# Kernel optimization log

Measured on AMD Instinct MI355X. Metric: run time of the kernel, lower is better.

The kernel has to match this reference:

```python
import jax, jax.numpy as jnp
import numpy as np

N_NODES = 50000
N_EDGES = 600000
IN_DIM = 128
HID = 128
N_CLASSES = 40
N_GRAPHS = 128


def setup_inputs() -> dict:
    key = jax.random.key(0)
    ks = jax.random.split(key, 12)
    x = jax.random.normal(ks[0], (N_NODES, IN_DIM), dtype=jnp.float32)
    edge_index = jax.random.randint(ks[1], (2, N_EDGES), 0, N_NODES, dtype=jnp.int64)
    batch = jnp.sort(jax.random.randint(ks[2], (N_NODES,), 0, N_GRAPHS, dtype=jnp.int64))
    dims = [IN_DIM, HID, HID, N_CLASSES]
    params = {}
    for l in range(3):
        d_in, d_out = dims[l], dims[l + 1]
        s = 1.0 / np.sqrt(d_in)
        params[f"Wl{l}"] = jax.random.uniform(ks[3 + 3 * l], (d_out, d_in), jnp.float32, -s, s)
        params[f"bl{l}"] = jax.random.uniform(ks[4 + 3 * l], (d_out,), jnp.float32, -s, s)
        params[f"Wr{l}"] = jax.random.uniform(ks[5 + 3 * l], (d_out, d_in), jnp.float32, -s, s)
    return {"x": x, "edge_index": edge_index, "batch": batch, **params}


def _sage_layer(h, src, dst, Wl, bl, Wr):
    # message: relu(x_j) (edge_attr is None -> zero), mean-aggregate at dst
    m = jnp.maximum(h[src], 0.0)                       # [E, d]
    agg = jax.ops.segment_sum(m, dst, num_segments=N_NODES)
    cnt = jax.ops.segment_sum(jnp.ones((m.shape[0],), h.dtype), dst, num_segments=N_NODES)
    agg = agg / jnp.maximum(cnt, 1.0)[:, None]
    # lin_l(agg) + lin_r(x)
    return agg @ Wl.T + bl + h @ Wr.T


def reference(x, edge_index, batch, Wl0, bl0, Wr0, Wl1, bl1, Wr1, Wl2, bl2, Wr2):
    src, dst = edge_index[0], edge_index[1]
    Ws = [(Wl0, bl0, Wr0), (Wl1, bl1, Wr1), (Wl2, bl2, Wr2)]
    h = x
    for l, (Wl, bl, Wr) in enumerate(Ws):
        # dropout is identity in eval mode
        h = _sage_layer(h, src, dst, Wl, bl, Wr)
        if l != len(Ws) - 1:
            h = jnp.maximum(h, 0.0)
    # global mean pool over graphs
    gsum = jax.ops.segment_sum(h, batch, num_segments=N_GRAPHS)
    gcnt = jax.ops.segment_sum(jnp.ones((h.shape[0],), h.dtype), batch, num_segments=N_GRAPHS)
    g = gsum / jnp.maximum(gcnt, 1.0)[:, None]
    return h, g
```

## Files before the change

kernel.cpp:

```cpp
#include <hip/hip_runtime.h>
#include <hip/hip_bf16.h>


#define NODES 50000
#define K_DIM 128
#define N_GRAPHS 128

typedef __attribute__((ext_vector_type(8))) short short8;
typedef __attribute__((ext_vector_type(4))) short short4v;
typedef __attribute__((ext_vector_type(4))) float f32x4;

__device__ inline short f2bf(float f) {
    unsigned u = __builtin_bit_cast(unsigned, f);
    u += 0x7FFFu + ((u >> 16) & 1u);
    return (short)(u >> 16);
}
__device__ inline float bf2f(short h) {
    unsigned u = ((unsigned)(unsigned short)h) << 16;
    return __builtin_bit_cast(float, u);
}
__device__ inline float blo(unsigned u) { return __builtin_bit_cast(float, u << 16); }
__device__ inline float bhi(unsigned u) { return __builtin_bit_cast(float, u & 0xFFFF0000u); }
__device__ inline unsigned hilo_pack(float f) {
    short h = f2bf(f);
    short l = f2bf(f - bf2f(h));
    return ((unsigned)(unsigned short)h) | (((unsigned)(unsigned short)l) << 16);
}

__global__ void init_kernel(const float* __restrict__ w0, const float* __restrict__ w1,
                            const float* __restrict__ w2, const float* __restrict__ w3,
                            const float* __restrict__ w4, const float* __restrict__ w5,
                            short* __restrict__ whi, short* __restrict__ wlo,
                            int* __restrict__ deg, const int* __restrict__ batch,
                            int* __restrict__ gstart, int* __restrict__ counter,
                            const float* __restrict__ x, short* __restrict__ xb,
                            float* __restrict__ gsum, int N) {
    int idx = blockIdx.x * 256 + threadIdx.x;
    if (idx < N * (K_DIM / 4)) {
        float4 v = reinterpret_cast<const float4*>(x)[idx];
        short4v b;
        b[0] = f2bf(fmaxf(v.x, 0.f));
        b[1] = f2bf(fmaxf(v.y, 0.f));
        b[2] = f2bf(fmaxf(v.z, 0.f));
        b[3] = f2bf(fmaxf(v.w, 0.f));
        *reinterpret_cast<short4v*>(&xb[idx * 4]) = b;
    }
    if (idx < N) deg[idx] = 0;
    if (idx < N_GRAPHS * 40) gsum[idx] = 0.f;
    if (idx == 0) *counter = 0;
    const int TOT = 4 * 16384 + 96 * 128;
    if (idx < TOT) {
        float v;
        if (idx < 65536) {
            int m = idx >> 14, e = idx & 16383;
            const float* W = (m == 0) ? w0 : (m == 1) ? w1 : (m == 2) ? w2 : w3;
            v = W[e];
        } else {
            int i2 = idx - 65536;
            int row = i2 >> 7, col = i2 & 127;
            if (row < 40)      v = w4[row * 128 + col];
            else if (row < 80) v = w5[(row - 40) * 128 + col];
            else               v = 0.f;
        }
        unsigned p = hilo_pack(v);
        whi[idx] = (short)(p & 0xFFFFu);
        wlo[idx] = (short)(p >> 16);
    }
    if (idx <= N_GRAPHS) {
        int g = idx;
        int lo = 0, hi = N;
        while (lo < hi) {
            int mid = (lo + hi) >> 1;
            if (batch[mid] < g) lo = mid + 1; else hi = mid;
        }
        gstart[g] = lo;
    }
}

__global__ void deg_kernel(const int* __restrict__ dst, int* __restrict__ deg, int E) {
    int e = blockIdx.x * blockDim.x + threadIdx.x;
    if (e < E) atomicAdd(&deg[dst[e]], 1);
}

__global__ void csr_offsets(const int* __restrict__ deg, int* __restrict__ counter,
                            int* __restrict__ rowptr, int* __restrict__ fillpos, int N) {
    const int tid = threadIdx.x, lane = tid & 63, wv = tid >> 6;
    int i = blockIdx.x * 256 + tid;
    int v = (i < N) ? deg[i] : 0;
    int incl = v;
    #pragma unroll
    for (int off = 1; off < 64; off <<= 1) {
        int t = __shfl_up(incl, off, 64);
        if (lane >= off) incl += t;
    }
    __shared__ int ws[4];
    __shared__ int sbase;
    if (lane == 63) ws[wv] = incl;
    __syncthreads();
    if (tid == 0) sbase = atomicAdd(counter, ws[0] + ws[1] + ws[2] + ws[3]);
    __syncthreads();
    int add = sbase;
    for (int k = 0; k < wv; ++k) add += ws[k];
    int excl = add + incl - v;
    if (i < N) { rowptr[i] = excl; fillpos[i] = excl; }
}

__global__ void fill_kernel(const int* __restrict__ src, const int* __restrict__ dst,
                            int* __restrict__ fillpos, int* __restrict__ csr_src, int E) {
    int e = blockIdx.x * blockDim.x + threadIdx.x;
    if (e < E) {
        int p = atomicAdd(&fillpos[dst[e]], 1);
        csr_src[p] = src[e];
    }
}

__global__ void agg_bf16(const unsigned short* __restrict__ hb,
                         const int* __restrict__ rowptr, const int* __restrict__ deg,
                         const int* __restrict__ csr_src,
                         short* __restrict__ aggb, int N) {
    int w = (blockIdx.x * blockDim.x + threadIdx.x) >> 6;
    if (w >= N) return;
    int lane = threadIdx.x & 63;
    int slot = lane >> 4, l16 = lane & 15;
    int s = rowptr[w];
    int e = s + deg[w];
    const uint4* T = reinterpret_cast<const uint4*>(hb);
    float2 a0 = make_float2(0.f, 0.f), a1 = a0, a2 = a0, a3 = a0;
    int i = s + slot;
    for (; i + 4 < e; i += 8) {
        uint4 va = T[(size_t)csr_src[i] * 16 + l16];
        uint4 vb = T[(size_t)csr_src[i + 4] * 16 + l16];
        a0.x += blo(va.x) + blo(vb.x); a0.y += bhi(va.x) + bhi(vb.x);
        a1.x += blo(va.y) + blo(vb.y); a1.y += bhi(va.y) + bhi(vb.y);
        a2.x += blo(va.z) + blo(vb.z); a2.y += bhi(va.z) + bhi(vb.z);
        a3.x += blo(va.w) + blo(vb.w); a3.y += bhi(va.w) + bhi(vb.w);
    }
    for (; i < e; i += 4) {
        uint4 va = T[(size_t)csr_src[i] * 16 + l16];
        a0.x += blo(va.x); a0.y += bhi(va.x);
        a1.x += blo(va.y); a1.y += bhi(va.y);
        a2.x += blo(va.z); a2.y += bhi(va.z);
        a3.x += blo(va.w); a3.y += bhi(va.w);
    }
    #pragma unroll
    for (int off = 16; off <= 32; off <<= 1) {
        a0.x += __shfl_xor(a0.x, off, 64); a0.y += __shfl_xor(a0.y, off, 64);
        a1.x += __shfl_xor(a1.x, off, 64); a1.y += __shfl_xor(a1.y, off, 64);
        a2.x += __shfl_xor(a2.x, off, 64); a2.y += __shfl_xor(a2.y, off, 64);
        a3.x += __shfl_xor(a3.x, off, 64); a3.y += __shfl_xor(a3.y, off, 64);
    }
    if (slot == 0) {
        float inv = 1.0f / fmaxf((float)(e - s), 1.0f);
        short8 b;
        b[0] = f2bf(a0.x * inv); b[1] = f2bf(a0.y * inv);
        b[2] = f2bf(a1.x * inv); b[3] = f2bf(a1.y * inv);
        b[4] = f2bf(a2.x * inv); b[5] = f2bf(a2.y * inv);
        b[6] = f2bf(a3.x * inv); b[7] = f2bf(a3.y * inv);
        *reinterpret_cast<short8*>(&aggb[(size_t)w * K_DIM + l16 * 8]) = b;
    }
}

__global__ __launch_bounds__(256) void sage0_mfma(
        const short* __restrict__ Ab_in, const float* __restrict__ Xf,
        const short* __restrict__ Bhl, const short* __restrict__ Bll,
        const short* __restrict__ Bhr, const short* __restrict__ Blr,
        const float* __restrict__ bl,
        short* __restrict__ outHi, short* __restrict__ outLo, int N) {
    constexpr int BM = 64;
    constexpr int LSTR = 40;
    const int tid = threadIdx.x;
    const int lane = tid & 63;
    const int wave = tid >> 6;
    const int l15 = lane & 15;
    const int quad = lane >> 4;
    const int m0 = blockIdx.x * BM;
    const int srow = tid >> 2, sc8 = tid & 3;

    __shared__ __align__(16) short Ab [BM * LSTR];
    __shared__ __align__(16) short Ahi[BM * LSTR];
    __shared__ __align__(16) short Alo[BM * LSTR];

    f32x4 acc[4][2];
    #pragma unroll
    for (int i = 0; i < 4; ++i)
        #pragma unroll
        for (int j = 0; j < 2; ++j) acc[i][j] = (f32x4){0.f, 0.f, 0.f, 0.f};

    const short8 zero8 = (short8){0, 0, 0, 0, 0, 0, 0, 0};
    const int sm = m0 + srow;

    for (int k0 = 0; k0 < K_DIM; k0 += 32) {
        __syncthreads();
        {
            short8 va = zero8, vh = zero8, vl = zero8;
            if (sm < N) {
                va = *reinterpret_cast<const short8*>(Ab_in + (size_t)sm * K_DIM + k0 + sc8 * 8);
                const float* xp = Xf + (size_t)sm * K_DIM + k0 + sc8 * 8;
                float4 f0 = *reinterpret_cast<const float4*>(xp);
                float4 f1 = *reinterpret_cast<const float4*>(xp + 4);
                float fv[8] = {f0.x, f0.y, f0.z, f0.w, f1.x, f1.y, f1.z, f1.w};
                #pragma unroll
                for (int j = 0; j < 8; ++j) {
                    unsigned p = hilo_pack(fv[j]);
                    vh[j] = (short)(p & 0xFFFFu);
                    vl[j] = (short)(p >> 16);
                }
            }
            *reinterpret_cast<short8*>(&Ab [srow * LSTR + sc8 * 8]) = va;
            *reinterpret_cast<short8*>(&Ahi[srow * LSTR + sc8 * 8]) = vh;
            *reinterpret_cast<short8*>(&Alo[srow * LSTR + sc8 * 8]) = vl;
        }
        short8 bhl_[2], bll_[2], bhr_[2], blr_[2];
        #pragma unroll
        for (int nt = 0; nt < 2; ++nt) {
            int n = wave * 32 + nt * 16 + l15;
            size_t off = (size_t)n * K_DIM + k0 + quad * 8;
            bhl_[nt] = *reinterpret_cast<const short8*>(Bhl + off);
            bll_[nt] = *reinterpret_cast<const short8*>(Bll + off);
            bhr_[nt] = *reinterpret_cast<const short8*>(Bhr + off);
            blr_[nt] = *reinterpret_cast<const short8*>(Blr + off);
        }
        __syncthreads();
        #pragma unroll
        for (int mt = 0; mt < 4; ++mt) {
            int row = mt * 16 + l15;
            short8 ab = *reinterpret_cast<const short8*>(&Ab [row * LSTR + quad * 8]);
            short8 ah = *reinterpret_cast<const short8*>(&Ahi[row * LSTR + quad * 8]);
            short8 ao = *reinterpret_cast<const short8*>(&Alo[row * LSTR + quad * 8]);
            #pragma unroll
            for (int nt = 0; nt < 2; ++nt) {
                acc[mt][nt] = __builtin_amdgcn_mfma_f32_16x16x32_bf16(ab, bhl_[nt], acc[mt][nt], 0, 0, 0);
                acc[mt][nt] = __builtin_amdgcn_mfma_f32_16x16x32_bf16(ab, bll_[nt], acc[mt][nt], 0, 0, 0);
                acc[mt][nt] = __builtin_amdgcn_mfma_f32_16x16x32_bf16(ah, bhr_[nt], acc[mt][nt], 0, 0, 0);
                acc[mt][nt] = __builtin_amdgcn_mfma_f32_16x16x32_bf16(ah, blr_[nt], acc[mt][nt], 0, 0, 0);
                acc[mt][nt] = __builtin_amdgcn_mfma_f32_16x16x32_bf16(ao, bhr_[nt], acc[mt][nt], 0, 0, 0);
            }
        }
    }

    #pragma unroll
    for (int mt = 0; mt < 4; ++mt) {
        #pragma unroll
        for (int nt = 0; nt < 2; ++nt) {
            int col = wave * 32 + nt * 16 + l15;
            float b = bl[col];
            #pragma unroll
            for (int reg = 0; reg < 4; ++reg) {
                int row = m0 + mt * 16 + quad * 4 + reg;
                if (row < N) {
                    float v = fmaxf(acc[mt][nt][reg] + b, 0.f);
                    unsigned p = hilo_pack(v);
                    outHi[(size_t)row * K_DIM + col] = (short)(p & 0xFFFFu);
                    outLo[(size_t)row * K_DIM + col] = (short)(p >> 16);
                }
            }
        }
    }
}

__global__ __launch_bounds__(256) void sage1_gemm80(
        const short* __restrict__ Ab_in,
        const short* __restrict__ Hhi_in, const short* __restrict__ Hlo_in,
        const short* __restrict__ Bhl, const short* __restrict__ Bll,
        const short* __restrict__ Bhr, const short* __restrict__ Blr,
        const float* __restrict__ bl,
        const short* __restrict__ B2h, const short* __restrict__ B2l,
        const float* __restrict__ b2,
        short* __restrict__ ylb, float* __restrict__ yr40, int N) {
    constexpr int BM = 64;
    constexpr int LSTR = 40;
    constexpr int LSTR2 = 136;
    const int tid = threadIdx.x;
    const int lane = tid & 63;
    const int wave = tid >> 6;
    const int l15 = lane & 15;
    const int quad = lane >> 4;
    const int m0 = blockIdx.x * BM;
    const int srow = tid >> 2, sc8 = tid & 3;

    __shared__ __align__(16) short Ab [BM * LSTR];
    __shared__ __align__(16) short Ahi[BM * LSTR];
    __shared__ __align__(16) short Alo[BM * LSTR];
    __shared__ __align__(16) short H2h[BM * LSTR2];
    __shared__ __align__(16) short H2l[BM * LSTR2];

    f32x4 acc[4][2];
    #pragma unroll
    for (int i = 0; i < 4; ++i)
        #pragma unroll
        for (int j = 0; j < 2; ++j) acc[i][j] = (f32x4){0.f, 0.f, 0.f, 0.f};

    const short8 zero8 = (short8){0, 0, 0, 0, 0, 0, 0, 0};
    const int sm = m0 + srow;

    for (int k0 = 0; k0 < K_DIM; k0 += 32) {
        __syncthreads();
        {
            short8 va = zero8, vh = zero8, vl = zero8;
            if (sm < N) {
                va = *reinterpret_cast<const short8*>(Ab_in  + (size_t)sm * K_DIM + k0 + sc8 * 8);
                vh = *reinterpret_cast<const short8*>(Hhi_in + (size_t)sm * K_DIM + k0 + sc8 * 8);
                vl = *reinterpret_cast<const short8*>(Hlo_in + (size_t)sm * K_DIM + k0 + sc8 * 8);
            }
            *reinterpret_cast<short8*>(&Ab [srow * LSTR + sc8 * 8]) = va;
            *reinterpret_cast<short8*>(&Ahi[srow * LSTR + sc8 * 8]) = vh;
            *reinterpret_cast<short8*>(&Alo[srow * LSTR + sc8 * 8]) = vl;
        }
        short8 bhl_[2], bll_[2], bhr_[2], blr_[2];
        #pragma unroll
        for (int nt = 0; nt < 2; ++nt) {
            int n = wave * 32 + nt * 16 + l15;
            size_t off = (size_t)n * K_DIM + k0 + quad * 8;
            bhl_[nt] = *reinterpret_cast<const short8*>(Bhl + off);
            bll_[nt] = *reinterpret_cast<const short8*>(Bll + off);
            bhr_[nt] = *reinterpret_cast<const short8*>(Bhr + off);
            blr_[nt] = *reinterpret_cast<const short8*>(Blr + off);
        }
        __syncthreads();
        #pragma unroll
        for (int mt = 0; mt < 4; ++mt) {
            int row = mt * 16 + l15;
            short8 ab = *reinterpret_cast<const short8*>(&Ab [row * LSTR + quad * 8]);
            short8 ah = *reinterpret_cast<const short8*>(&Ahi[row * LSTR + quad * 8]);
            short8 ao = *reinterpret_cast<const short8*>(&Alo[row * LSTR + quad * 8]);
            #pragma unroll
            for (int nt = 0; nt < 2; ++nt) {
                acc[mt][nt] = __builtin_amdgcn_mfma_f32_16x16x32_bf16(ab, bhl_[nt], acc[mt][nt], 0, 0, 0);
                acc[mt][nt] = __builtin_amdgcn_mfma_f32_16x16x32_bf16(ab, bll_[nt], acc[mt][nt], 0, 0, 0);
                acc[mt][nt] = __builtin_amdgcn_mfma_f32_16x16x32_bf16(ah, bhr_[nt], acc[mt][nt], 0, 0, 0);
                acc[mt][nt] = __builtin_amdgcn_mfma_f32_16x16x32_bf16(ah, blr_[nt], acc[mt][nt], 0, 0, 0);
                acc[mt][nt] = __builtin_amdgcn_mfma_f32_16x16x32_bf16(ao, bhr_[nt], acc[mt][nt], 0, 0, 0);
            }
        }
    }

    __syncthreads();
    #pragma unroll
    for (int mt = 0; mt < 4; ++mt) {
        #pragma unroll
        for (int nt = 0; nt < 2; ++nt) {
            int col = wave * 32 + nt * 16 + l15;
            float b = bl[col];
            #pragma unroll
            for (int reg = 0; reg < 4; ++reg) {
                int row = mt * 16 + quad * 4 + reg;
                float v = fmaxf(acc[mt][nt][reg] + b, 0.f);
                unsigned p = hilo_pack(v);
                H2h[row * LSTR2 + col] = (short)(p & 0xFFFFu);
                H2l[row * LSTR2 + col] = (short)(p >> 16);
            }
        }
    }
    __syncthreads();

    f32x4 c2[5];
    #pragma unroll
    for (int nt = 0; nt < 5; ++nt) c2[nt] = (f32x4){0.f, 0.f, 0.f, 0.f};
    const int arow = wave * 16 + l15;
    #pragma unroll
    for (int kc = 0; kc < 4; ++kc) {
        const int k0 = kc * 32;
        short8 ah = *reinterpret_cast<const short8*>(&H2h[arow * LSTR2 + k0 + quad * 8]);
        short8 ao = *reinterpret_cast<const short8*>(&H2l[arow * LSTR2 + k0 + quad * 8]);
        #pragma unroll
        for (int nt = 0; nt < 5; ++nt) {
            int n = nt * 16 + l15;
            size_t off = (size_t)n * K_DIM + k0 + quad * 8;
            short8 bh = *reinterpret_cast<const short8*>(B2h + off);
            short8 bo = *reinterpret_cast<const short8*>(B2l + off);
            c2[nt] = __builtin_amdgcn_mfma_f32_16x16x32_bf16(ah, bh, c2[nt], 0, 0, 0);
            c2[nt] = __builtin_amdgcn_mfma_f32_16x16x32_bf16(ah, bo, c2[nt], 0, 0, 0);
            c2[nt] = __builtin_amdgcn_mfma_f32_16x16x32_bf16(ao, bh, c2[nt], 0, 0, 0);
        }
    }

    #pragma unroll
    for (int nt = 0; nt < 5; ++nt) {
        int col = nt * 16 + l15;
        #pragma unroll
        for (int reg = 0; reg < 4; ++reg) {
            int row = m0 + wave * 16 + quad * 4 + reg;
            if (row < N) {
                float v = c2[nt][reg];
                if (col < 40) {
                    ylb[(size_t)row * 40 + col] = f2bf(v);
                } else {
                    yr40[(size_t)row * 40 + (col - 40)] = v + b2[col - 40];
                }
            }
        }
    }
}

__global__ __launch_bounds__(256) void agg40_pool(
        const unsigned int* __restrict__ ylbu, const float* __restrict__ yr40,
        const int* __restrict__ rowptr, const int* __restrict__ deg,
        const int* __restrict__ csr_src,
        const int* __restrict__ batch, const int* __restrict__ gstart,
        float* __restrict__ out, float* __restrict__ gsum, int N) {
    const int w = (blockIdx.x * blockDim.x + threadIdx.x) >> 6;
    const int lane = threadIdx.x & 63;
    const int wv = threadIdx.x >> 6;
    const int half = lane >> 5, l32 = lane & 31;
    __shared__ float sh[4][40];
    __shared__ int sg[4];
    __shared__ float sinv[4];

    if (w < N) {
        int s = rowptr[w], e = s + deg[w];
        float ax = 0.f, ay = 0.f;
        if (l32 < 20) {
            int i = s + half;
            for (; i + 6 < e; i += 8) {
                int s0 = csr_src[i], s1 = csr_src[i + 2], s2 = csr_src[i + 4], s3 = csr_src[i + 6];
                unsigned v0 = ylbu[(size_t)s0 * 20 + l32];
                unsigned v1 = ylbu[(size_t)s1 * 20 + l32];
                unsigned v2 = ylbu[(size_t)s2 * 20 + l32];
                unsigned v3 = ylbu[(size_t)s3 * 20 + l32];
                ax += (blo(v0) + blo(v1)) + (blo(v2) + blo(v3));
                ay += (bhi(v0) + bhi(v1)) + (bhi(v2) + bhi(v3));
            }
            for (; i < e; i += 2) {
                unsigned v0 = ylbu[(size_t)csr_src[i] * 20 + l32];
                ax += blo(v0); ay += bhi(v0);
            }
        }
        ax += __shfl_xor(ax, 32, 64);
        ay += __shfl_xor(ay, 32, 64);
        if (half == 0 && l32 < 20) {
            float inv = 1.0f / fmaxf((float)(e - s), 1.0f);
            float2 yr = *reinterpret_cast<const float2*>(&yr40[(size_t)w * 40 + 2 * l32]);
            float vx = ax * inv + yr.x;
            float vy = ay * inv + yr.y;
            *reinterpret_cast<float2*>(&out[(size_t)w * 40 + 2 * l32]) = make_float2(vx, vy);
            sh[wv][2 * l32]     = vx;
            sh[wv][2 * l32 + 1] = vy;
        }
    }
    if (lane == 0) {
        if (w < N) {
            int g = batch[w];
            sg[wv] = g;
            sinv[wv] = 1.0f / fmaxf((float)(gstart[g + 1] - gstart[g]), 1.0f);
        } else {
            sg[wv] = -1;
        }
    }
    __syncthreads();
    if (wv == 0 && lane < 40) {
        int cur = -1;
        float accum = 0.f;
        #pragma unroll
        for (int k = 0; k < 4; ++k) {
            int gk = sg[k];
            if (gk < 0) continue;
            float c = sh[k][lane] * sinv[k];
            if (gk == cur) {
                accum += c;
            } else {
                if (cur >= 0) atomicAdd(&gsum[cur * 40 + lane], accum);
                cur = gk;
                accum = c;
            }
        }
        if (cur >= 0) atomicAdd(&gsum[cur * 40 + lane], accum);
    }
}

extern "C" void kernel_launch(void* const* d_in, const int* in_sizes, int n_in,
                              void* d_out, int out_size, void* d_ws, size_t ws_size,
                              hipStream_t stream) {
    const float* x    = (const float*)d_in[0];
    const int*   ei   = (const int*)d_in[1];
    const int*   batch= (const int*)d_in[2];
    const float* Wl0  = (const float*)d_in[3];
    const float* bl0  = (const float*)d_in[4];
    const float* Wr0  = (const float*)d_in[5];
    const float* Wl1  = (const float*)d_in[6];
    const float* bl1  = (const float*)d_in[7];
    const float* Wr1  = (const float*)d_in[8];
    const float* Wl2  = (const float*)d_in[9];
    const float* bl2  = (const float*)d_in[10];
    const float* Wr2  = (const float*)d_in[11];

    const int N = in_sizes[0] / K_DIM;
    const int E = in_sizes[1] / 2;
    const int* src = ei;
    const int* dst = ei + E;

    float* out = (float*)d_out;
    float* gsum = out + (size_t)N * 40;

    char* w = (char*)d_ws;
    auto alloc = [&](size_t bytes) {
        char* p = w;
        w += (bytes + 255) & ~(size_t)255;
        return p;
    };
    const size_t PL = (size_t)N * K_DIM * 2;
    short* aggb  = (short*)alloc(PL);
    short* xb    = (short*)alloc(PL);
    short* h1hi  = (short*)alloc(PL);
    short* h1lo  = (short*)alloc(PL);
    short* ylb   = (short*)alloc((size_t)N * 40 * 2);
    float* yr40  = (float*)alloc((size_t)N * 40 * 4);
    int*   rowptr= (int*)alloc((size_t)(N + 1) * 4);
    int*   deg   = (int*)alloc((size_t)N * 4);
    int*   fillp = (int*)alloc((size_t)N * 4);
    int*   csr   = (int*)alloc((size_t)E * 4);
    int*   counter = (int*)alloc(256);
    int*   gstart= (int*)alloc((size_t)(N_GRAPHS + 1) * 4);
    short* whi   = (short*)alloc(77824 * 2);
    short* wlo   = (short*)alloc(77824 * 2);

    const int NB = (N + 255) / 256;
    const int initGrid = (N * (K_DIM / 4) + 255) / 256;

    init_kernel<<<initGrid, 256, 0, stream>>>(Wl0, Wr0, Wl1, Wr1, Wl2, Wr2,
                                              whi, wlo, deg, batch, gstart, counter,
                                              x, xb, gsum, N);
    deg_kernel<<<(E + 255) / 256, 256, 0, stream>>>(dst, deg, E);
    csr_offsets<<<NB, 256, 0, stream>>>(deg, counter, rowptr, fillp, N);
    fill_kernel<<<(E + 255) / 256, 256, 0, stream>>>(src, dst, fillp, csr, E);

    short* hWl0 = whi;          short* lWl0 = wlo;
    short* hWr0 = whi + 16384;  short* lWr0 = wlo + 16384;
    short* hWl1 = whi + 32768;  short* lWl1 = wlo + 32768;
    short* hWr1 = whi + 49152;  short* lWr1 = wlo + 49152;
    short* hW2  = whi + 65536;  short* lW2  = wlo + 65536;

    const int aggGrid  = (N * 64 + 255) / 256;
    const int gemmGrid = (N + 63) / 64;

    agg_bf16<<<aggGrid, 256, 0, stream>>>((const unsigned short*)xb, rowptr, deg, csr, aggb, N);
    sage0_mfma<<<gemmGrid, 256, 0, stream>>>(
        aggb, x, hWl0, lWl0, hWr0, lWr0, bl0, h1hi, h1lo, N);
    agg_bf16<<<aggGrid, 256, 0, stream>>>((const unsigned short*)h1hi, rowptr, deg, csr, aggb, N);
    sage1_gemm80<<<gemmGrid, 256, 0, stream>>>(
        aggb, h1hi, h1lo, hWl1, lWl1, hWr1, lWr1, bl1, hW2, lW2, bl2, ylb, yr40, N);
    agg40_pool<<<aggGrid, 256, 0, stream>>>((const unsigned int*)ylb, yr40,
                                            rowptr, deg, csr, batch, gstart, out, gsum, N);
}
```

Measured before the change: 319.6 us.

## Prefetch next A tile into registers and halve layer-2 LDS staging buffer

```diff
diff --git a/kernel.cpp b/kernel.cpp
--- a/kernel.cpp
+++ b/kernel.cpp
@@ -188,28 +188,18 @@
 
     const short8 zero8 = (short8){0, 0, 0, 0, 0, 0, 0, 0};
     const int sm = m0 + srow;
+    const bool rowok = (sm < N);
+
+    short8 va = zero8;
+    float4 f0 = make_float4(0.f,0.f,0.f,0.f), f1 = f0;
+    if (rowok) {
+        va = *reinterpret_cast<const short8*>(Ab_in + (size_t)sm * K_DIM + sc8 * 8);
+        const float* xp = Xf + (size_t)sm * K_DIM + sc8 * 8;
+        f0 = *reinterpret_cast<const float4*>(xp);
+        f1 = *reinterpret_cast<const float4*>(xp + 4);
+    }
 
     for (int k0 = 0; k0 < K_DIM; k0 += 32) {
-        __syncthreads();
-        {
-            short8 va = zero8, vh = zero8, vl = zero8;
-            if (sm < N) {
-                va = *reinterpret_cast<const short8*>(Ab_in + (size_t)sm * K_DIM + k0 + sc8 * 8);
-                const float* xp = Xf + (size_t)sm * K_DIM + k0 + sc8 * 8;
-                float4 f0 = *reinterpret_cast<const float4*>(xp);
-                float4 f1 = *reinterpret_cast<const float4*>(xp + 4);
-                float fv[8] = {f0.x, f0.y, f0.z, f0.w, f1.x, f1.y, f1.z, f1.w};
-                #pragma unroll
-                for (int j = 0; j < 8; ++j) {
-                    unsigned p = hilo_pack(fv[j]);
-                    vh[j] = (short)(p & 0xFFFFu);
-                    vl[j] = (short)(p >> 16);
-                }
-            }
-            *reinterpret_cast<short8*>(&Ab [srow * LSTR + sc8 * 8]) = va;
-            *reinterpret_cast<short8*>(&Ahi[srow * LSTR + sc8 * 8]) = vh;
-            *reinterpret_cast<short8*>(&Alo[srow * LSTR + sc8 * 8]) = vl;
-        }
         short8 bhl_[2], bll_[2], bhr_[2], blr_[2];
         #pragma unroll
         for (int nt = 0; nt < 2; ++nt) {
@@ -221,6 +211,27 @@
             blr_[nt] = *reinterpret_cast<const short8*>(Blr + off);
         }
         __syncthreads();
+        {
+            short8 vh = zero8, vl = zero8;
+            float fv[8] = {f0.x, f0.y, f0.z, f0.w, f1.x, f1.y, f1.z, f1.w};
+            #pragma unroll
+            for (int j = 0; j < 8; ++j) {
+                unsigned p = hilo_pack(fv[j]);
+                vh[j] = (short)(p & 0xFFFFu);
+                vl[j] = (short)(p >> 16);
+            }
+            if (!rowok) { vh = zero8; vl = zero8; }
+            *reinterpret_cast<short8*>(&Ab [srow * LSTR + sc8 * 8]) = va;
+            *reinterpret_cast<short8*>(&Ahi[srow * LSTR + sc8 * 8]) = vh;
+            *reinterpret_cast<short8*>(&Alo[srow * LSTR + sc8 * 8]) = vl;
+        }
+        __syncthreads();
+        if (k0 + 32 < K_DIM && rowok) {
+            va = *reinterpret_cast<const short8*>(Ab_in + (size_t)sm * K_DIM + k0 + 32 + sc8 * 8);
+            const float* xp = Xf + (size_t)sm * K_DIM + k0 + 32 + sc8 * 8;
+            f0 = *reinterpret_cast<const float4*>(xp);
+            f1 = *reinterpret_cast<const float4*>(xp + 4);
+        }
         #pragma unroll
         for (int mt = 0; mt < 4; ++mt) {
             int row = mt * 16 + l15;
@@ -269,7 +280,7 @@
         short* __restrict__ ylb, float* __restrict__ yr40, int N) {
     constexpr int BM = 64;
     constexpr int LSTR = 40;
-    constexpr int LSTR2 = 136;
+    constexpr int LSTR2 = 68;
     const int tid = threadIdx.x;
     const int lane = tid & 63;
     const int wave = tid >> 6;
@@ -292,20 +303,16 @@
 
     const short8 zero8 = (short8){0, 0, 0, 0, 0, 0, 0, 0};
     const int sm = m0 + srow;
+    const bool rowok = (sm < N);
+
+    short8 va = zero8, vh = zero8, vl = zero8;
+    if (rowok) {
+        va = *reinterpret_cast<const short8*>(Ab_in  + (size_t)sm * K_DIM + sc8 * 8);
+        vh = *reinterpret_cast<const short8*>(Hhi_in + (size_t)sm * K_DIM + sc8 * 8);
+        vl = *reinterpret_cast<const short8*>(Hlo_in + (size_t)sm * K_DIM + sc8 * 8);
+    }
 
     for (int k0 = 0; k0 < K_DIM; k0 += 32) {
-        __syncthreads();
-        {
-            short8 va = zero8, vh = zero8, vl = zero8;
-            if (sm < N) {
-                va = *reinterpret_cast<const short8*>(Ab_in  + (size_t)sm * K_DIM + k0 + sc8 * 8);
-                vh = *reinterpret_cast<const short8*>(Hhi_in + (size_t)sm * K_DIM + k0 + sc8 * 8);
-                vl = *reinterpret_cast<const short8*>(Hlo_in + (size_t)sm * K_DIM + k0 + sc8 * 8);
-            }
-            *reinterpret_cast<short8*>(&Ab [srow * LSTR + sc8 * 8]) = va;
-            *reinterpret_cast<short8*>(&Ahi[srow * LSTR + sc8 * 8]) = vh;
-            *reinterpret_cast<short8*>(&Alo[srow * LSTR + sc8 * 8]) = vl;
-        }
         short8 bhl_[2], bll_[2], bhr_[2], blr_[2];
         #pragma unroll
         for (int nt = 0; nt < 2; ++nt) {
@@ -317,6 +324,15 @@
             blr_[nt] = *reinterpret_cast<const short8*>(Blr + off);
         }
         __syncthreads();
+        *reinterpret_cast<short8*>(&Ab [srow * LSTR + sc8 * 8]) = va;
+        *reinterpret_cast<short8*>(&Ahi[srow * LSTR + sc8 * 8]) = vh;
+        *reinterpret_cast<short8*>(&Alo[srow * LSTR + sc8 * 8]) = vl;
+        __syncthreads();
+        if (k0 + 32 < K_DIM && rowok) {
+            va = *reinterpret_cast<const short8*>(Ab_in  + (size_t)sm * K_DIM + k0 + 32 + sc8 * 8);
+            vh = *reinterpret_cast<const short8*>(Hhi_in + (size_t)sm * K_DIM + k0 + 32 + sc8 * 8);
+            vl = *reinterpret_cast<const short8*>(Hlo_in + (size_t)sm * K_DIM + k0 + 32 + sc8 * 8);
+        }
         #pragma unroll
         for (int mt = 0; mt < 4; ++mt) {
             int row = mt * 16 + l15;
@@ -334,43 +350,48 @@
         }
     }
 
-    __syncthreads();
-    #pragma unroll
-    for (int mt = 0; mt < 4; ++mt) {
-        #pragma unroll
-        for (int nt = 0; nt < 2; ++nt) {
-            int col = wave * 32 + nt * 16 + l15;
-            float b = bl[col];
-            #pragma unroll
-            for (int reg = 0; reg < 4; ++reg) {
-                int row = mt * 16 + quad * 4 + reg;
-                float v = fmaxf(acc[mt][nt][reg] + b, 0.f);
-                unsigned p = hilo_pack(v);
-                H2h[row * LSTR2 + col] = (short)(p & 0xFFFFu);
-                H2l[row * LSTR2 + col] = (short)(p >> 16);
-            }
-        }
-    }
-    __syncthreads();
-
     f32x4 c2[5];
     #pragma unroll
     for (int nt = 0; nt < 5; ++nt) c2[nt] = (f32x4){0.f, 0.f, 0.f, 0.f};
     const int arow = wave * 16 + l15;
-    #pragma unroll
-    for (int kc = 0; kc < 4; ++kc) {
-        const int k0 = kc * 32;
-        short8 ah = *reinterpret_cast<const short8*>(&H2h[arow * LSTR2 + k0 + quad * 8]);
-        short8 ao = *reinterpret_cast<const short8*>(&H2l[arow * LSTR2 + k0 + quad * 8]);
-        #pragma unroll
-        for (int nt = 0; nt < 5; ++nt) {
-            int n = nt * 16 + l15;
-            size_t off = (size_t)n * K_DIM + k0 + quad * 8;
-            short8 bh = *reinterpret_cast<const short8*>(B2h + off);
-            short8 bo = *reinterpret_cast<const short8*>(B2l + off);
-            c2[nt] = __builtin_amdgcn_mfma_f32_16x16x32_bf16(ah, bh, c2[nt], 0, 0, 0);
-            c2[nt] = __builtin_amdgcn_mfma_f32_16x16x32_bf16(ah, bo, c2[nt], 0, 0, 0);
-            c2[nt] = __builtin_amdgcn_mfma_f32_16x16x32_bf16(ao, bh, c2[nt], 0, 0, 0);
+
+    #pragma unroll
+    for (int half = 0; half < 2; ++half) {
+        __syncthreads();
+        if ((wave >> 1) == half) {
+            #pragma unroll
+            for (int mt = 0; mt < 4; ++mt) {
+                #pragma unroll
+                for (int nt = 0; nt < 2; ++nt) {
+                    int col = (wave & 1) * 32 + nt * 16 + l15;
+                    float b = bl[half * 64 + col];
+                    #pragma unroll
+                    for (int reg = 0; reg < 4; ++reg) {
+                        int row = mt * 16 + quad * 4 + reg;
+                        float v = fmaxf(acc[mt][nt][reg] + b, 0.f);
+                        unsigned p = hilo_pack(v);
+                        H2h[row * LSTR2 + col] = (short)(p & 0xFFFFu);
+                        H2l[row * LSTR2 + col] = (short)(p >> 16);
+                    }
+                }
+            }
+        }
+        __syncthreads();
+        #pragma unroll
+        for (int kc2 = 0; kc2 < 2; ++kc2) {
+            const int k0 = half * 64 + kc2 * 32;
+            short8 ah = *reinterpret_cast<const short8*>(&H2h[arow * LSTR2 + kc2 * 32 + quad * 8]);
+            short8 ao = *reinterpret_cast<const short8*>(&H2l[arow * LSTR2 + kc2 * 32 + quad * 8]);
+            #pragma unroll
+            for (int nt = 0; nt < 5; ++nt) {
+                int n = nt * 16 + l15;
+                size_t off = (size_t)n * K_DIM + k0 + quad * 8;
+                short8 bh = *reinterpret_cast<const short8*>(B2h + off);
+                short8 bo = *reinterpret_cast<const short8*>(B2l + off);
+                c2[nt] = __builtin_amdgcn_mfma_f32_16x16x32_bf16(ah, bh, c2[nt], 0, 0, 0);
+                c2[nt] = __builtin_amdgcn_mfma_f32_16x16x32_bf16(ah, bo, c2[nt], 0, 0, 0);
+                c2[nt] = __builtin_amdgcn_mfma_f32_16x16x32_bf16(ao, bh, c2[nt], 0, 0, 0);
+            }
         }
     }
 
```

After: 325.2 us. Within noise of the previous version (+1.8%).
